# Performance work log

Hardware: AMD Instinct MI355X
Metric: run time of the kernel (lower is better)

## Reference

```python
import jax, jax.numpy as jnp
import numpy as np

C = 256            # in_channels
SHIFTS = (1, 2, 3, 4)
S = len(SHIFTS)
HID = C // S       # 64
H = W = 64
AREA = H * W
EPS = 1e-5
NORM_EPS = 1e-12
# offsets (dy, dx) encoded by the 8 one-hot 3x3 kernels (kernels 1..8)
OFFSETS = [(-1,-1), (-1,0), (-1,1), (0,1), (1,1), (1,0), (1,-1), (0,-1)]


def shift2d(x, dy, dx):
    # x: [b, c, H, W]; out[y, x] = x[y+dy, x+dx], zeros outside (== dilated depthwise conv with one-hot kernel)
    d = max(abs(dy), abs(dx), 1)
    xp = jnp.pad(x, ((0,0),(0,0),(d,d),(d,d)))
    return xp[:, :, d+dy:d+dy+x.shape[2], d+dx:d+dx+x.shape[3]]


def setup_inputs() -> dict:
    key = jax.random.key(0)
    ks = jax.random.split(key, 8)
    sd = 0.02
    return {
        "cen": jax.random.normal(ks[0], (4, C, H, W), dtype=jnp.float32),
        "query_w": jax.random.normal(ks[1], (S, HID, C), dtype=jnp.float32) * sd,
        "local_w": jax.random.normal(ks[2], (S, HID, C), dtype=jnp.float32) * sd,
        "key_w":   jax.random.normal(ks[3], (S, 8*HID, 8*C), dtype=jnp.float32) * sd,
        "value_w": jax.random.normal(ks[4], (S, 8*HID, 8*C), dtype=jnp.float32) * sd,
        "out_w":   jax.random.normal(ks[5], (C, C), dtype=jnp.float32) * sd,
        "bn_gamma": jnp.ones((C,), dtype=jnp.float32),
        "bn_beta":  jnp.zeros((C,), dtype=jnp.float32),
    }


def reference(cen, query_w, local_w, key_w, value_w, out_w, bn_gamma, bn_beta):
    b, _, h, w = cen.shape
    cenf = cen.reshape(b, C, AREA)
    keys, qs, vals, locs = [], [], [], []
    for i, d in enumerate(SHIFTS):
        # gather 8 dilated neighbors -> [b, 8C, area]
        surr = jnp.concatenate([shift2d(cen, dy*d, dx*d) for dy, dx in OFFSETS], axis=1)
        surr = surr.reshape(b, 8*C, AREA)
        keys.append(jnp.einsum('oc,bca->boa', key_w[i], surr))
        vals.append(jnp.einsum('oc,bca->boa', value_w[i], surr))
        qs.append(jnp.einsum('oc,bca->boa', query_w[i], cenf))
        locs.append(jnp.einsum('oc,bca->boa', local_w[i], cenf))
    keys = jnp.stack(keys, 1)   # [b,S,8h,area]
    vals = jnp.stack(vals, 1)   # [b,S,8h,area]
    qs   = jnp.stack(qs, 1)     # [b,S,h,area]
    locs = jnp.stack(locs, 1)   # [b,S,h,area]

    # L2 normalize over area (torch F.normalize: x / max(||x||, eps))
    kn = keys / jnp.maximum(jnp.linalg.norm(keys, axis=-1, keepdims=True), NORM_EPS)
    qn = qs   / jnp.maximum(jnp.linalg.norm(qs,   axis=-1, keepdims=True), NORM_EPS)

    # channel attention: contract over area -> [b,S,h,8h]
    score = jnp.einsum('bsha,bska->bshk', qn, kn)
    # InstanceNorm2d over (h, 8h) per (b, S), affine=False, biased var
    mu = score.mean(axis=(-2,-1), keepdims=True)
    var = score.var(axis=(-2,-1), keepdims=True)
    score = (score - mu) * jax.lax.rsqrt(var + EPS)
    ws = jax.nn.softmax(score, axis=-1)                     # [b,S,h,8h]
    wc = ws.reshape(b, S, HID, 8, HID).sum(axis=3)          # sum of 8 chunks -> [b,S,h,h]

    out = jnp.einsum('bshk,bska->bsha', ws, vals) - jnp.einsum('bshk,bska->bsha', wc, locs)
    out = out.reshape(b, C, h, w)

    # out_conv: 1x1 conv -> BatchNorm2d (training stats, biased var) -> ReLU
    out = jnp.einsum('oc,bchw->bohw', out_w, out)
    m = out.mean(axis=(0,2,3), keepdims=True)
    v = out.var(axis=(0,2,3), keepdims=True)
    out = (out - m) * jax.lax.rsqrt(v + EPS)
    out = out * bn_gamma[None, :, None, None] + bn_beta[None, :, None, None]
    return jax.nn.relu(out)
```

## Files before the change

kernel.cpp:

```cpp
#include <hip/hip_runtime.h>


typedef unsigned short u16;
typedef unsigned int u32;
typedef __attribute__((ext_vector_type(4))) unsigned int u32x4;
typedef __attribute__((ext_vector_type(8))) short s16x8;
typedef __attribute__((ext_vector_type(4))) float f32x4;

#define DEVFN static __device__ __forceinline__

DEVFN u16 f2bf(float f) {
    u32 u = __builtin_bit_cast(u32, f);
    u32 r = (u + 0x7fffu + ((u >> 16) & 1u)) >> 16;
    return (u16)r;
}
DEVFN float bf2f(u32 h) { u32 u = h << 16; return __builtin_bit_cast(float, u); }

typedef __attribute__((address_space(1))) const unsigned int gu32;
typedef __attribute__((address_space(3))) unsigned int lu32;
DEVFN void gld16(const void* g, void* l) {
    __builtin_amdgcn_global_load_lds((gu32*)g, (lu32*)l, 16, 0, 0);
}

__constant__ int cOFFY[8] = {-1,-1,-1, 0, 1, 1, 1, 0};
__constant__ int cOFFX[8] = {-1, 0, 1, 1, 1, 0,-1,-1};

#define CENROWS 4097

DEVFN int swz(int r, int kb) { return r * 128 + (kb ^ ((r & 7) << 4)); }

template<int BM, int BN, int WRM, int WRN, int XG, int YG, int DM, int NRM, int KSP, int SWZ>
__global__ __launch_bounds__(256, 2)
void gemm_tn(const u16* __restrict__ X, const u16* __restrict__ Y,
             void* __restrict__ D, const u16* __restrict__ cenT,
             float* __restrict__ nrm,
             int K, int ldx, int ldy, int ldd, int sbits,
             long xb, long xs, long yb, long ys, long db, long dsn,
             long nb, long ns, long kpl)
{
    static_assert(KSP == 1 || (!XG && !YG), "split-K only for non-gather");
    int bx = blockIdx.x, by = blockIdx.y, bz = blockIdx.z;
    if constexpr (SWZ) {
        const int gx = gridDim.x, gy = gridDim.y;
        const int nwg = gx * gy * (int)gridDim.z;
        const int flat = bx + gx * (by + gy * bz);
        const int r = (flat & 7) * (nwg >> 3) + (flat >> 3);
        bx = r % gx; by = (r / gx) % gy; bz = r / (gx * gy);
    }
    const int tid  = threadIdx.x;
    const int lane = tid & 63;
    const int wid  = tid >> 6;
    const int b = bz >> sbits;
    const int s = bz & ((1 << sbits) - 1);
    const int m0 = bx * BM;
    const int ksl = (KSP > 1) ? (by % KSP) : 0;
    const int n0 = (KSP > 1 ? (by / KSP) : by) * BN;
    const int koff = ksl * (K / KSP);
    const int dil = s + 1;
    const int wm0 = (wid >> 1) * (WRM * 16);
    const int wn0 = (wid & 1) * (WRN * 16);

    __shared__ __align__(16) char lds[2 * (BM + BN) * 128];

    const char* cenB = (const char*)(cenT + (long)b * (CENROWS * 256));
    const char* Xb = nullptr;
    const char* Yb = nullptr;
    if constexpr (!XG) Xb = (const char*)(X + b * xb + (long)s * xs + (long)m0 * ldx + koff);
    if constexpr (!YG) Yb = (const char*)(Y + b * yb + (long)s * ys + (long)n0 * ldy + koff);

    u32 offX[XG ? BM / 32 : 1];
    u32 offY[YG ? BN / 32 : 1];
    auto calcOff = [&](int j) {
        const int dy = (j < 8) ? cOFFY[j] * dil : 0;
        const int dx = (j < 8) ? cOFFX[j] * dil : 0;
        if constexpr (XG) {
            #pragma unroll
            for (int r = 0; r < BM / 32; r++) {
                const int R = r * 32 + wid * 8 + (lane >> 3);
                const int a = m0 + R, yy = (a >> 6) + dy, xx = (a & 63) + dx;
                const int row = (((unsigned)yy < 64u) && ((unsigned)xx < 64u)) ? ((yy << 6) + xx) : 4096;
                offX[r] = ((u32)row << 9) + (((lane & 7) * 16) ^ ((R & 7) << 4));
            }
        }
        if constexpr (YG) {
            #pragma unroll
            for (int r = 0; r < BN / 32; r++) {
                const int R = r * 32 + wid * 8 + (lane >> 3);
                const int a = n0 + R, yy = (a >> 6) + dy, xx = (a & 63) + dx;
                const int row = (((unsigned)yy < 64u) && ((unsigned)xx < 64u)) ? ((yy << 6) + xx) : 4096;
                offY[r] = ((u32)row << 9) + (((lane & 7) * 16) ^ ((R & 7) << 4));
            }
        }
    };

    auto stage = [&](int bf, int t) {
        char* LX = lds + bf * ((BM + BN) * 128);
        char* LY = LX + BM * 128;
        if constexpr (!XG) {
            const char* base = Xb + (long)t * 128;
            #pragma unroll
            for (int r = 0; r < BM / 32; r++) {
                const int R = r * 32 + wid * 8 + (lane >> 3);
                gld16(base + (long)R * (ldx * 2) + (((lane & 7) * 16) ^ ((R & 7) << 4)),
                      LX + (r * 32 + wid * 8) * 128);
            }
        } else {
            const int cb = (t & 3) * 128;
            #pragma unroll
            for (int r = 0; r < BM / 32; r++)
                gld16(cenB + offX[r] + cb, LX + (r * 32 + wid * 8) * 128);
        }
        if constexpr (!YG) {
            const char* base = Yb + (long)t * 128;
            #pragma unroll
            for (int r = 0; r < BN / 32; r++) {
                const int R = r * 32 + wid * 8 + (lane >> 3);
                gld16(base + (long)R * (ldy * 2) + (((lane & 7) * 16) ^ ((R & 7) << 4)),
                      LY + (r * 32 + wid * 8) * 128);
            }
        } else {
            const int cb = (t & 3) * 128;
            #pragma unroll
            for (int r = 0; r < BN / 32; r++)
                gld16(cenB + offY[r] + cb, LY + (r * 32 + wid * 8) * 128);
        }
    };

    f32x4 acc[WRM][WRN] = {};

    auto comp = [&](int bf) {
        const char* LX = lds + bf * ((BM + BN) * 128);
        const char* LY = LX + BM * 128;
        #pragma unroll
        for (int kk = 0; kk < 2; kk++) {
            const int kb = kk * 64 + ((lane >> 4) << 4);
            s16x8 af[WRM], bfr[WRN];
            #pragma unroll
            for (int m = 0; m < WRM; m++)
                af[m] = *(const s16x8*)(LX + swz(wm0 + m * 16 + (lane & 15), kb));
            #pragma unroll
            for (int n = 0; n < WRN; n++)
                bfr[n] = *(const s16x8*)(LY + swz(wn0 + n * 16 + (lane & 15), kb));
            #pragma unroll
            for (int m = 0; m < WRM; m++)
                #pragma unroll
                for (int n = 0; n < WRN; n++)
                    acc[m][n] = __builtin_amdgcn_mfma_f32_16x16x32_bf16(af[m], bfr[n], acc[m][n], 0, 0, 0);
        }
    };

    const int nt = (K / KSP) / 64;
    if constexpr (XG || YG) calcOff(0);
    stage(0, 0);
    __syncthreads();
    int cur = 0;
    for (int t = 0; t < nt; t++) {
        if (t + 1 < nt) {
            if constexpr (XG || YG) {
                if (((t + 1) & 3) == 0) calcOff((t + 1) >> 2);
            }
            stage(cur ^ 1, t + 1);
        }
        comp(cur);
        __syncthreads();
        cur ^= 1;
    }

    if constexpr (NRM) {
        const int slot = (by << 1) + (wid & 1);
        #pragma unroll
        for (int m = 0; m < WRM; m++) {
            float ss[4] = {0.f, 0.f, 0.f, 0.f};
            float s1v[4] = {0.f, 0.f, 0.f, 0.f};
            #pragma unroll
            for (int n = 0; n < WRN; n++)
                #pragma unroll
                for (int i = 0; i < 4; i++) {
                    float v = (NRM == 1) ? bf2f(f2bf(acc[m][n][i])) : acc[m][n][i];
                    ss[i] += v * v;
                    if constexpr (NRM == 2) s1v[i] += v;
                }
            #pragma unroll
            for (int o = 1; o < 16; o <<= 1)
                #pragma unroll
                for (int i = 0; i < 4; i++) {
                    ss[i] += __shfl_xor(ss[i], o);
                    if constexpr (NRM == 2) s1v[i] += __shfl_xor(s1v[i], o);
                }
            if ((lane & 15) == 0) {
                const int row0 = m0 + wm0 + m * 16 + ((lane >> 4) << 2);
                #pragma unroll
                for (int i = 0; i < 4; i++) {
                    if constexpr (NRM == 1) {
                        nrm[((long)(b * nb + s * ns + row0 + i) << 6) + slot] = ss[i];
                    } else {
                        float* p = nrm + ((long)(row0 + i) << 8) + (b << 6) + slot;
                        p[0] = s1v[i];
                        p[65536] = ss[i];
                    }
                }
            }
        }
    }

    #pragma unroll
    for (int m = 0; m < WRM; m++) {
        const int row0 = m0 + wm0 + m * 16 + ((lane >> 4) << 2);
        #pragma unroll
        for (int n = 0; n < WRN; n++) {
            const int col = n0 + wn0 + n * 16 + (lane & 15);
            f32x4 a = acc[m][n];
            if constexpr (DM == 1) {
                float* Dp = (float*)D + (long)ksl * kpl + b * db + (long)s * dsn;
                #pragma unroll
                for (int i = 0; i < 4; i++) Dp[(long)(row0 + i) * ldd + col] = a[i];
            } else {
                u16* Dp = (u16*)D + b * db + (long)s * dsn;
                #pragma unroll
                for (int i = 0; i < 4; i++) Dp[(long)(row0 + i) * ldd + col] = f2bf(a[i]);
            }
        }
    }
}

__global__ void cast_all(const float* __restrict__ kw, const float* __restrict__ qw,
                         const float* __restrict__ ow,
                         u16* __restrict__ KWb, u16* __restrict__ QWb,
                         u16* __restrict__ OWb, u16* __restrict__ cenT) {
    const int i = blockIdx.x * 256 + threadIdx.x;
    const float* src; u16* dst; long o;
    if (i < 524288)      { src = kw; dst = KWb; o = i; }
    else if (i < 532480) { src = qw; dst = QWb; o = i - 524288; }
    else if (i < 540672) { src = ow; dst = OWb; o = i - 532480; }
    else {
        const int t = (i - 540672) * 1;
        if (t < 512) {
            const int b = t >> 7, w = t & 127;
            ((u32*)(cenT + (long)b * (CENROWS * 256) + 4096L * 256))[w] = 0u;
        }
        return;
    }
    const float* s = src + o * 8;
    u32x4 v;
    #pragma unroll
    for (int j = 0; j < 4; j++) {
        u16 lo = f2bf(s[2 * j]), hi = f2bf(s[2 * j + 1]);
        v[j] = (u32)lo | ((u32)hi << 16);
    }
    *(u32x4*)(dst + o * 8) = v;
}

__global__ __launch_bounds__(256) void transpose_cast(const float* __restrict__ src, u16* __restrict__ dst,
                                                      int R, int C, float scale, long dstride) {
    __shared__ float t[64][65];
    const int tx = threadIdx.x & 63, ty = threadIdx.x >> 6;
    const int c0 = blockIdx.x * 64, r0 = blockIdx.y * 64;
    const float* s = src + (long)blockIdx.z * R * C + (long)r0 * C + c0;
    #pragma unroll
    for (int i = 0; i < 16; i++) t[ty + i * 4][tx] = s[(long)(ty + i * 4) * C + tx];
    __syncthreads();
    u16* d = dst + (long)blockIdx.z * dstride + (long)c0 * R + r0;
    #pragma unroll
    for (int i = 0; i < 16; i++) d[(long)(ty + i * 4) * R + tx] = f2bf(t[tx][ty + i * 4] * scale);
}

__global__ __launch_bounds__(1024) void softmax_in(const float* __restrict__ score,
                                                   const float* __restrict__ nQp,
                                                   const float* __restrict__ nKp,
                                                   u16* __restrict__ wswc) {
    constexpr long PL = 524288;
    const int bs = blockIdx.x, tid = threadIdx.x;
    const int b = bs >> 2, s = bs & 3;
    const float* S = score + (long)bs * 32768;
    __shared__ float invq[64], invk[512];
    if (tid < 64) {
        const float* p = nQp + ((long)(b * 256 + s * 64 + tid) << 6);
        float a = 0.f;
        #pragma unroll
        for (int j = 0; j < 64; j++) a += p[j];
        invq[tid] = 1.f / fmaxf(sqrtf(a), 1e-12f);
    }
    if (tid < 512) {
        const float* p = nKp + (((long)bs * 512 + tid) << 6);
        float a = 0.f;
        #pragma unroll
        for (int j = 0; j < 64; j++) a += p[j];
        invk[tid] = 1.f / fmaxf(sqrtf(a), 1e-12f);
    }
    __syncthreads();
    auto ldS = [&](int i) -> float {
        return S[i] + S[i + PL] + S[i + 2 * PL] + S[i + 3 * PL];
    };
    float s1 = 0.f, s2 = 0.f;
    for (int i = tid; i < 32768; i += 1024) {
        float v = ldS(i) * invq[i >> 9] * invk[i & 511];
        s1 += v; s2 += v * v;
    }
    __shared__ float ra[1024], rb[1024];
    ra[tid] = s1; rb[tid] = s2; __syncthreads();
    for (int st = 512; st > 0; st >>= 1) {
        if (tid < st) { ra[tid] += ra[tid + st]; rb[tid] += rb[tid + st]; }
        __syncthreads();
    }
    const float mu = ra[0] * (1.f / 32768.f);
    const float var = rb[0] * (1.f / 32768.f) - mu * mu;
    const float rstd = rsqrtf(var + 1e-5f);
    const int wid = tid >> 6, lane = tid & 63;
    u16* W = wswc + (long)bs * 64 * 576;
    for (int r = wid; r < 64; r += 16) {
        float zv[8]; float mx = -3.0e38f;
        const float iq = invq[r];
        #pragma unroll
        for (int i = 0; i < 8; i++) {
            const int c = i * 64 + lane;
            zv[i] = (ldS(r * 512 + c) * iq * invk[c] - mu) * rstd;
            mx = fmaxf(mx, zv[i]);
        }
        #pragma unroll
        for (int o = 32; o > 0; o >>= 1) mx = fmaxf(mx, __shfl_xor(mx, o));
        float sum = 0.f;
        #pragma unroll
        for (int i = 0; i < 8; i++) { zv[i] = __expf(zv[i] - mx); sum += zv[i]; }
        #pragma unroll
        for (int o = 32; o > 0; o >>= 1) sum += __shfl_xor(sum, o);
        const float inv = 1.f / sum;
        float wcv = 0.f;
        #pragma unroll
        for (int i = 0; i < 8; i++) {
            float w = zv[i] * inv; wcv += w;
            W[r * 576 + i * 64 + lane] = f2bf(w);
        }
        W[r * 576 + 512 + lane] = f2bf(wcv);
    }
}

__global__ __launch_bounds__(256) void bn_finalize(const float* __restrict__ bnp,
                                                   const float* __restrict__ gamma,
                                                   const float* __restrict__ beta,
                                                   float* __restrict__ st) {
    const int c = threadIdx.x;
    const float* p = bnp + ((long)c << 8);
    float s1 = 0.f, s2 = 0.f;
    #pragma unroll 8
    for (int j = 0; j < 256; j++) { s1 += p[j]; s2 += p[65536 + j]; }
    const float mu = s1 * (1.f / 16384.f);
    const float var = s2 * (1.f / 16384.f) - mu * mu;
    const float g = gamma[c] * rsqrtf(var + 1e-5f);
    st[c * 2] = g;
    st[c * 2 + 1] = beta[c] - mu * g;
}

__global__ __launch_bounds__(256) void bn_apply(const u16* __restrict__ out2b,
                                                const float* __restrict__ st,
                                                float* __restrict__ out) {
    const long i8 = (long)blockIdx.x * 256 + threadIdx.x;
    const u32x4 v = *(const u32x4*)(out2b + i8 * 8);
    const int c = (int)((i8 * 8) >> 12) & 255;
    const float g = st[c * 2], bt = st[c * 2 + 1];
    float* o = out + i8 * 8;
    #pragma unroll
    for (int j = 0; j < 4; j++) {
        o[2 * j]     = fmaxf(bf2f(v[j] & 0xffff) * g + bt, 0.f);
        o[2 * j + 1] = fmaxf(bf2f(v[j] >> 16) * g + bt, 0.f);
    }
}

extern "C" void kernel_launch(void* const* d_in, const int* in_sizes, int n_in,
                              void* d_out, int out_size, void* d_ws, size_t ws_size,
                              hipStream_t stream) {
    (void)in_sizes; (void)n_in; (void)out_size; (void)ws_size;
    const float* cen   = (const float*)d_in[0];
    const float* qw    = (const float*)d_in[1];
    const float* lw    = (const float*)d_in[2];
    const float* kw    = (const float*)d_in[3];
    const float* vw    = (const float*)d_in[4];
    const float* ow    = (const float*)d_in[5];
    const float* gamma = (const float*)d_in[6];
    const float* beta  = (const float*)d_in[7];
    float* out = (float*)d_out;

    char* ws = (char*)d_ws;
    size_t off = 0;
    auto alloc = [&](size_t bytes) { size_t o = off; off += (bytes + 255) & ~(size_t)255; return o; };
    u16*   KWb   = (u16*)(ws + alloc(4L * 512 * 2048 * 2));
    u16*   VWt   = (u16*)(ws + alloc(4L * 2048 * 512 * 2));
    u16*   QWb   = (u16*)(ws + alloc(256L * 256 * 2));
    u16*   LWt   = (u16*)(ws + alloc(4L * 256 * 64 * 2));
    u16*   OWb   = (u16*)(ws + alloc(256L * 256 * 2));
    u16*   cenT  = (u16*)(ws + alloc(4L * CENROWS * 256 * 2));
    u16*   keys  = (u16*)(ws + alloc(16L * 512 * 4096 * 2));
    u16*   qs    = (u16*)(ws + alloc(16L * 64 * 4096 * 2));
    float* score = (float*)(ws + alloc(4L * 16 * 64 * 512 * 4));
    u16*   WSWC  = (u16*)(ws + alloc(16L * 64 * 576 * 2));
    u16*   Xcomb = (u16*)(ws + alloc(16L * 64 * 2304 * 2));
    u16*   out1t = (u16*)(ws + alloc(4L * 4096 * 256 * 2));
    u16*   out2b = (u16*)(ws + alloc(4L * 256 * 4096 * 2));
    float* bnst  = (float*)(ws + alloc(256L * 2 * 4));
    float* nKp   = (float*)(ws + alloc(16L * 512 * 64 * 4));
    float* nQp   = (float*)(ws + alloc(4L * 256 * 64 * 4));
    float* bnp   = (float*)(ws + alloc(2L * 65536 * 4));

    cast_all<<<dim3(2115), 256, 0, stream>>>(kw, qw, ow, KWb, QWb, OWb, cenT);
    transpose_cast<<<dim3(32, 8, 4), 256, 0, stream>>>(vw, VWt, 512, 2048, 1.f, 512L * 2048);
    transpose_cast<<<dim3(4, 1, 4),  256, 0, stream>>>(lw, LWt, 64, 256, -1.f, 64L * 256);
    transpose_cast<<<dim3(64, 4, 4), 256, 0, stream>>>(cen, cenT, 256, 4096, 1.f, (long)CENROWS * 256);

    gemm_tn<128,128,4,4, 0,1, 0, 1, 1, 1><<<dim3(4, 32, 16), 256, 0, stream>>>(
        KWb, nullptr, keys, cenT, nKp,
        2048, 2048, 0, 4096, 2,
        0L, 512L * 2048, 0L, 0L, 4L * 512 * 4096, 512L * 4096, 2048L, 512L, 0L);
    gemm_tn<64,128,2,4, 0,0, 0, 1, 1, 0><<<dim3(4, 32, 4), 256, 0, stream>>>(
        QWb, cenT, qs, cenT, nQp,
        256, 256, 256, 4096, 0,
        0L, 0L, (long)CENROWS * 256, 0L, 256L * 4096, 0L, 256L, 0L, 0L);
    gemm_tn<64,64,2,2, 0,0, 1, 0, 4, 0><<<dim3(1, 32, 16), 256, 0, stream>>>(
        qs, keys, score, cenT, nullptr,
        4096, 4096, 4096, 512, 2,
        256L * 4096, 64L * 4096, 4L * 512 * 4096, 512L * 4096, 4L * 64 * 512, 64L * 512,
        0L, 0L, 524288L);
    softmax_in<<<dim3(16), 1024, 0, stream>>>(score, nQp, nKp, WSWC);

    gemm_tn<64,128,2,4, 0,0, 0, 0, 1, 0><<<dim3(1, 16, 16), 256, 0, stream>>>(
        WSWC, VWt, Xcomb, cenT, nullptr,
        512, 576, 512, 2304, 2,
        4L * 64 * 576, 64L * 576, 0L, 2048L * 512, 4L * 64 * 2304, 64L * 2304, 0L, 0L, 0L);
    gemm_tn<64,128,2,4, 0,0, 0, 0, 1, 0><<<dim3(1, 2, 16), 256, 0, stream>>>(
        WSWC + 512, LWt, Xcomb + 2048, cenT, nullptr,
        64, 576, 64, 2304, 2,
        4L * 64 * 576, 64L * 576, 0L, 256L * 64, 4L * 64 * 2304, 64L * 2304, 0L, 0L, 0L);
    gemm_tn<128,64,4,2, 1,0, 0, 0, 1, 1><<<dim3(32, 1, 16), 256, 0, stream>>>(
        nullptr, Xcomb, out1t, cenT, nullptr,
        2304, 0, 2304, 256, 2,
        0L, 0L, 4L * 64 * 2304, 64L * 2304, 4096L * 256, 64L, 0L, 0L, 0L);

    gemm_tn<64,128,2,4, 0,0, 0, 2, 1, 0><<<dim3(4, 32, 4), 256, 0, stream>>>(
        OWb, out1t, out2b, cenT, bnp,
        256, 256, 256, 4096, 0,
        0L, 0L, 4096L * 256, 0L, 256L * 4096, 0L, 0L, 0L, 0L);

    bn_finalize<<<dim3(1), 256, 0, stream>>>(bnp, gamma, beta, bnst);
    bn_apply<<<dim3(2048), 256, 0, stream>>>(out2b, bnst, out);
}
```

Baseline: 280.6 us.

## Use 512-thread blocks for key GEMM and fuse prep kernels into one

The large gathered key GEMM now runs with 512 threads (8 waves) per 128x128 tile. Each wave holds a 4x2 fragment instead of 4x4, and the launch bound allows 4 blocks per CU. The per-row norm partials grow to 128 slots, and the softmax kernel sums 128 entries to match. Separately, the four weight and input cast/transpose kernels merge into a single prep_all launch to cut launch overhead. The aim is more latency hiding and fewer launches, at the cost of halved register-level reuse per wave and more norm-partial traffic.

```diff
diff --git a/kernel.cpp b/kernel.cpp
--- a/kernel.cpp
+++ b/kernel.cpp
@@ -29,8 +29,9 @@
 
 DEVFN int swz(int r, int kb) { return r * 128 + (kb ^ ((r & 7) << 4)); }
 
-template<int BM, int BN, int WRM, int WRN, int XG, int YG, int DM, int NRM, int KSP, int SWZ>
-__global__ __launch_bounds__(256, 2)
+template<int BM, int BN, int WRM, int WRN, int XG, int YG, int DM, int NRM,
+         int KSP, int SWZ, int THREADS, int NSH>
+__global__ __launch_bounds__(THREADS, (THREADS == 512 ? 4 : 2))
 void gemm_tn(const u16* __restrict__ X, const u16* __restrict__ Y,
              void* __restrict__ D, const u16* __restrict__ cenT,
              float* __restrict__ nrm,
@@ -39,6 +40,8 @@
              long nb, long ns, long kpl)
 {
     static_assert(KSP == 1 || (!XG && !YG), "split-K only for non-gather");
+    constexpr int NWN = (THREADS == 512) ? 4 : 2;
+    constexpr int TPR = THREADS / 8;
     int bx = blockIdx.x, by = blockIdx.y, bz = blockIdx.z;
     if constexpr (SWZ) {
         const int gx = gridDim.x, gy = gridDim.y;
@@ -57,8 +60,8 @@
     const int n0 = (KSP > 1 ? (by / KSP) : by) * BN;
     const int koff = ksl * (K / KSP);
     const int dil = s + 1;
-    const int wm0 = (wid >> 1) * (WRM * 16);
-    const int wn0 = (wid & 1) * (WRN * 16);
+    const int wm0 = (wid / NWN) * (WRM * 16);
+    const int wn0 = (wid % NWN) * (WRN * 16);
 
     __shared__ __align__(16) char lds[2 * (BM + BN) * 128];
 
@@ -68,15 +71,15 @@
     if constexpr (!XG) Xb = (const char*)(X + b * xb + (long)s * xs + (long)m0 * ldx + koff);
     if constexpr (!YG) Yb = (const char*)(Y + b * yb + (long)s * ys + (long)n0 * ldy + koff);
 
-    u32 offX[XG ? BM / 32 : 1];
-    u32 offY[YG ? BN / 32 : 1];
+    u32 offX[XG ? BM / TPR : 1];
+    u32 offY[YG ? BN / TPR : 1];
     auto calcOff = [&](int j) {
         const int dy = (j < 8) ? cOFFY[j] * dil : 0;
         const int dx = (j < 8) ? cOFFX[j] * dil : 0;
         if constexpr (XG) {
             #pragma unroll
-            for (int r = 0; r < BM / 32; r++) {
-                const int R = r * 32 + wid * 8 + (lane >> 3);
+            for (int r = 0; r < BM / TPR; r++) {
+                const int R = r * TPR + (tid >> 3);
                 const int a = m0 + R, yy = (a >> 6) + dy, xx = (a & 63) + dx;
                 const int row = (((unsigned)yy < 64u) && ((unsigned)xx < 64u)) ? ((yy << 6) + xx) : 4096;
                 offX[r] = ((u32)row << 9) + (((lane & 7) * 16) ^ ((R & 7) << 4));
@@ -84,8 +87,8 @@
         }
         if constexpr (YG) {
             #pragma unroll
-            for (int r = 0; r < BN / 32; r++) {
-                const int R = r * 32 + wid * 8 + (lane >> 3);
+            for (int r = 0; r < BN / TPR; r++) {
+                const int R = r * TPR + (tid >> 3);
                 const int a = n0 + R, yy = (a >> 6) + dy, xx = (a & 63) + dx;
                 const int row = (((unsigned)yy < 64u) && ((unsigned)xx < 64u)) ? ((yy << 6) + xx) : 4096;
                 offY[r] = ((u32)row << 9) + (((lane & 7) * 16) ^ ((R & 7) << 4));
@@ -99,30 +102,30 @@
         if constexpr (!XG) {
             const char* base = Xb + (long)t * 128;
             #pragma unroll
-            for (int r = 0; r < BM / 32; r++) {
-                const int R = r * 32 + wid * 8 + (lane >> 3);
+            for (int r = 0; r < BM / TPR; r++) {
+                const int R = r * TPR + (tid >> 3);
                 gld16(base + (long)R * (ldx * 2) + (((lane & 7) * 16) ^ ((R & 7) << 4)),
-                      LX + (r * 32 + wid * 8) * 128);
+                      LX + (r * TPR + wid * 8) * 128);
             }
         } else {
             const int cb = (t & 3) * 128;
             #pragma unroll
-            for (int r = 0; r < BM / 32; r++)
-                gld16(cenB + offX[r] + cb, LX + (r * 32 + wid * 8) * 128);
+            for (int r = 0; r < BM / TPR; r++)
+                gld16(cenB + offX[r] + cb, LX + (r * TPR + wid * 8) * 128);
         }
         if constexpr (!YG) {
             const char* base = Yb + (long)t * 128;
             #pragma unroll
-            for (int r = 0; r < BN / 32; r++) {
-                const int R = r * 32 + wid * 8 + (lane >> 3);
+            for (int r = 0; r < BN / TPR; r++) {
+                const int R = r * TPR + (tid >> 3);
                 gld16(base + (long)R * (ldy * 2) + (((lane & 7) * 16) ^ ((R & 7) << 4)),
-                      LY + (r * 32 + wid * 8) * 128);
+                      LY + (r * TPR + wid * 8) * 128);
             }
         } else {
             const int cb = (t & 3) * 128;
             #pragma unroll
-            for (int r = 0; r < BN / 32; r++)
-                gld16(cenB + offY[r] + cb, LY + (r * 32 + wid * 8) * 128);
+            for (int r = 0; r < BN / TPR; r++)
+                gld16(cenB + offY[r] + cb, LY + (r * TPR + wid * 8) * 128);
         }
     };
 
@@ -167,7 +170,7 @@
     }
 
     if constexpr (NRM) {
-        const int slot = (by << 1) + (wid & 1);
+        const int slot = by * NWN + (wid % NWN);
         #pragma unroll
         for (int m = 0; m < WRM; m++) {
             float ss[4] = {0.f, 0.f, 0.f, 0.f};
@@ -192,7 +195,7 @@
                 #pragma unroll
                 for (int i = 0; i < 4; i++) {
                     if constexpr (NRM == 1) {
-                        nrm[((long)(b * nb + s * ns + row0 + i) << 6) + slot] = ss[i];
+                        nrm[((long)(b * nb + s * ns + row0 + i) << NSH) + slot] = ss[i];
                     } else {
                         float* p = nrm + ((long)(row0 + i) << 8) + (b << 6) + slot;
                         p[0] = s1v[i];
@@ -223,43 +226,62 @@
     }
 }
 
-__global__ void cast_all(const float* __restrict__ kw, const float* __restrict__ qw,
-                         const float* __restrict__ ow,
-                         u16* __restrict__ KWb, u16* __restrict__ QWb,
-                         u16* __restrict__ OWb, u16* __restrict__ cenT) {
-    const int i = blockIdx.x * 256 + threadIdx.x;
-    const float* src; u16* dst; long o;
-    if (i < 524288)      { src = kw; dst = KWb; o = i; }
-    else if (i < 532480) { src = qw; dst = QWb; o = i - 524288; }
-    else if (i < 540672) { src = ow; dst = OWb; o = i - 532480; }
-    else {
-        const int t = (i - 540672) * 1;
-        if (t < 512) {
-            const int b = t >> 7, w = t & 127;
-            ((u32*)(cenT + (long)b * (CENROWS * 256) + 4096L * 256))[w] = 0u;
-        }
+__global__ __launch_bounds__(256) void prep_all(
+    const float* __restrict__ kw, const float* __restrict__ qw,
+    const float* __restrict__ ow, const float* __restrict__ vw,
+    const float* __restrict__ lw, const float* __restrict__ cen,
+    u16* __restrict__ KWb, u16* __restrict__ QWb, u16* __restrict__ OWb,
+    u16* __restrict__ VWt, u16* __restrict__ LWt, u16* __restrict__ cenT)
+{
+    const int bid = blockIdx.x;
+    const int tid = threadIdx.x;
+    __shared__ float t[64][65];
+
+    if (bid < 2112) {
+        const float* src; u16* dst; long o;
+        const long i = (long)bid * 256 + tid;
+        if (bid < 2048)      { src = kw; dst = KWb; o = i; }
+        else if (bid < 2080) { src = qw; dst = QWb; o = i - 2048L * 256; }
+        else                 { src = ow; dst = OWb; o = i - 2080L * 256; }
+        const float* s = src + o * 8;
+        u32x4 v;
+        #pragma unroll
+        for (int j = 0; j < 4; j++) {
+            u16 lo = f2bf(s[2 * j]), hi = f2bf(s[2 * j + 1]);
+            v[j] = (u32)lo | ((u32)hi << 16);
+        }
+        *(u32x4*)(dst + o * 8) = v;
         return;
     }
-    const float* s = src + o * 8;
-    u32x4 v;
+    if (bid == 4176) {
+        if (tid < 128)
+            #pragma unroll
+            for (int b2 = 0; b2 < 4; b2++)
+                ((u32*)(cenT + (long)b2 * (CENROWS * 256) + 4096L * 256))[tid] = 0u;
+        return;
+    }
+    const float* src; u16* dst; int R, C; float scale; long dstride;
+    int cx, ry, z;
+    int tb = bid - 2112;
+    if (tb < 1024) {
+        src = vw; dst = VWt; R = 512; C = 2048; scale = 1.f; dstride = 512L * 2048;
+        cx = tb & 31; ry = (tb >> 5) & 7; z = tb >> 8;
+    } else if (tb < 1040) {
+        tb -= 1024;
+        src = lw; dst = LWt; R = 64; C = 256; scale = -1.f; dstride = 64L * 256;
+        cx = tb & 3; ry = 0; z = tb >> 2;
+    } else {
+        tb -= 1040;
+        src = cen; dst = cenT; R = 256; C = 4096; scale = 1.f; dstride = (long)CENROWS * 256;
+        cx = tb & 63; ry = (tb >> 6) & 3; z = tb >> 8;
+    }
+    const int tx = tid & 63, ty = tid >> 6;
+    const int c0 = cx * 64, r0 = ry * 64;
+    const float* sp = src + (long)z * R * C + (long)r0 * C + c0;
     #pragma unroll
-    for (int j = 0; j < 4; j++) {
-        u16 lo = f2bf(s[2 * j]), hi = f2bf(s[2 * j + 1]);
-        v[j] = (u32)lo | ((u32)hi << 16);
-    }
-    *(u32x4*)(dst + o * 8) = v;
-}
-
-__global__ __launch_bounds__(256) void transpose_cast(const float* __restrict__ src, u16* __restrict__ dst,
-                                                      int R, int C, float scale, long dstride) {
-    __shared__ float t[64][65];
-    const int tx = threadIdx.x & 63, ty = threadIdx.x >> 6;
-    const int c0 = blockIdx.x * 64, r0 = blockIdx.y * 64;
-    const float* s = src + (long)blockIdx.z * R * C + (long)r0 * C + c0;
-    #pragma unroll
-    for (int i = 0; i < 16; i++) t[ty + i * 4][tx] = s[(long)(ty + i * 4) * C + tx];
+    for (int i = 0; i < 16; i++) t[ty + i * 4][tx] = sp[(long)(ty + i * 4) * C + tx];
     __syncthreads();
-    u16* d = dst + (long)blockIdx.z * dstride + (long)c0 * R + r0;
+    u16* d = dst + (long)z * dstride + (long)c0 * R + r0;
     #pragma unroll
     for (int i = 0; i < 16; i++) d[(long)(ty + i * 4) * R + tx] = f2bf(t[tx][ty + i * 4] * scale);
 }
@@ -281,10 +303,10 @@
         invq[tid] = 1.f / fmaxf(sqrtf(a), 1e-12f);
     }
     if (tid < 512) {
-        const float* p = nKp + (((long)bs * 512 + tid) << 6);
+        const float* p = nKp + (((long)bs * 512 + tid) << 7);
         float a = 0.f;
         #pragma unroll
-        for (int j = 0; j < 64; j++) a += p[j];
+        for (int j = 0; j < 128; j++) a += p[j];
         invk[tid] = 1.f / fmaxf(sqrtf(a), 1e-12f);
     }
     __syncthreads();
@@ -396,44 +418,42 @@
     u16*   out1t = (u16*)(ws + alloc(4L * 4096 * 256 * 2));
     u16*   out2b = (u16*)(ws + alloc(4L * 256 * 4096 * 2));
     float* bnst  = (float*)(ws + alloc(256L * 2 * 4));
-    float* nKp   = (float*)(ws + alloc(16L * 512 * 64 * 4));
+    float* nKp   = (float*)(ws + alloc(16L * 512 * 128 * 4));
     float* nQp   = (float*)(ws + alloc(4L * 256 * 64 * 4));
     float* bnp   = (float*)(ws + alloc(2L * 65536 * 4));
 
-    cast_all<<<dim3(2115), 256, 0, stream>>>(kw, qw, ow, KWb, QWb, OWb, cenT);
-    transpose_cast<<<dim3(32, 8, 4), 256, 0, stream>>>(vw, VWt, 512, 2048, 1.f, 512L * 2048);
-    transpose_cast<<<dim3(4, 1, 4),  256, 0, stream>>>(lw, LWt, 64, 256, -1.f, 64L * 256);
-    transpose_cast<<<dim3(64, 4, 4), 256, 0, stream>>>(cen, cenT, 256, 4096, 1.f, (long)CENROWS * 256);
-
-    gemm_tn<128,128,4,4, 0,1, 0, 1, 1, 1><<<dim3(4, 32, 16), 256, 0, stream>>>(
+    prep_all<<<dim3(4177), 256, 0, stream>>>(kw, qw, ow, vw, lw, cen,
+                                             KWb, QWb, OWb, VWt, LWt, cenT);
+
+    gemm_tn<128,128,4,2, 0,1, 0, 1, 1, 1, 512, 7><<<dim3(4, 32, 16), 512, 0, stream>>>(
         KWb, nullptr, keys, cenT, nKp,
         2048, 2048, 0, 4096, 2,
         0L, 512L * 2048, 0L, 0L, 4L * 512 * 4096, 512L * 4096, 2048L, 512L, 0L);
-    gemm_tn<64,128,2,4, 0,0, 0, 1, 1, 0><<<dim3(4, 32, 4), 256, 0, stream>>>(
+    gemm_tn<64,128,2,4, 0,0, 0, 1, 1, 0, 256, 6><<<dim3(4, 32, 4), 256, 0, stream>>>(
         QWb, cenT, qs, cenT, nQp,
         256, 256, 256, 4096, 0,
         0L, 0L, (long)CENROWS * 256, 0L, 256L * 4096, 0L, 256L, 0L, 0L);
-    gemm_tn<64,64,2,2, 0,0, 1, 0, 4, 0><<<dim3(1, 32, 16), 256, 0, stream>>>(
+    gemm_tn<64,64,2,2, 0,0, 1, 0, 4, 0, 256, 6><<<dim3(1, 32, 16), 256, 0, stream>>>(
         qs, keys, score, cenT, nullptr,
         4096, 4096, 4096, 512, 2,
         256L * 4096, 64L * 4096, 4L * 512 * 4096, 512L * 4096, 4L * 64 * 512, 64L * 512,
         0L, 0L, 524288L);
     softmax_in<<<dim3(16), 1024, 0, stream>>>(score, nQp, nKp, WSWC);
 
-    gemm_tn<64,128,2,4, 0,0, 0, 0, 1, 0><<<dim3(1, 16, 16), 256, 0, stream>>>(
+    gemm_tn<64,128,2,4, 0,0, 0, 0, 1, 0, 256, 6><<<dim3(1, 16, 16), 256, 0, stream>>>(
         WSWC, VWt, Xcomb, cenT, nullptr,
         512, 576, 512, 2304, 2,
         4L * 64 * 576, 64L * 576, 0L, 2048L * 512, 4L * 64 * 2304, 64L * 2304, 0L, 0L, 0L);
-    gemm_tn<64,128,2,4, 0,0, 0, 0, 1, 0><<<dim3(1, 2, 16), 256, 0, stream>>>(
+    gemm_tn<64,128,2,4, 0,0, 0, 0, 1, 0, 256, 6><<<dim3(1, 2, 16), 256, 0, stream>>>(
         WSWC + 512, LWt, Xcomb + 2048, cenT, nullptr,
         64, 576, 64, 2304, 2,
         4L * 64 * 576, 64L * 576, 0L, 256L * 64, 4L * 64 * 2304, 64L * 2304, 0L, 0L, 0L);
-    gemm_tn<128,64,4,2, 1,0, 0, 0, 1, 1><<<dim3(32, 1, 16), 256, 0, stream>>>(
+    gemm_tn<128,64,4,2, 1,0, 0, 0, 1, 1, 256, 6><<<dim3(32, 1, 16), 256, 0, stream>>>(
         nullptr, Xcomb, out1t, cenT, nullptr,
         2304, 0, 2304, 256, 2,
         0L, 0L, 4L * 64 * 2304, 64L * 2304, 4096L * 256, 64L, 0L, 0L, 0L);
 
-    gemm_tn<64,128,2,4, 0,0, 0, 2, 1, 0><<<dim3(4, 32, 4), 256, 0, stream>>>(
+    gemm_tn<64,128,2,4, 0,0, 0, 2, 1, 0, 256, 6><<<dim3(4, 32, 4), 256, 0, stream>>>(
         OWb, out1t, out2b, cenT, bnp,
         256, 256, 256, 4096, 0,
         0L, 0L, 4096L * 256, 0L, 256L * 4096, 0L, 0L, 0L, 0L);
```

Measured after the change: 280.5 us, median of 2. About the same (-0.0%).
